# Kernel optimization log

Hardware: AMD Instinct MI355X
Metric: run time of the kernel (lower is better)

Reference implementation:

```python
import jax, jax.numpy as jnp
import numpy as np
from jax import lax


def haar_dwt2(x):
    """Single-level 2D Haar (db1) DWT matching pywt sign conventions.
    x: (..., H, W) with H, W even. Returns (cA, cH, cV, cD) each (..., H/2, W/2).
    pywt db1: approx = (x0+x1)/sqrt2, detail = (x0-x1)/sqrt2; dwt2 keys:
    cH='da' (detail axis -2), cV='ad' (detail axis -1).
    """
    a = x[..., 0::2, 0::2]
    b = x[..., 0::2, 1::2]
    c = x[..., 1::2, 0::2]
    d = x[..., 1::2, 1::2]
    cA = (a + b + c + d) * 0.5
    cH = (a + b - c - d) * 0.5
    cV = (a - b + c - d) * 0.5
    cD = (a - b - c + d) * 0.5
    return cA, cH, cV, cD


def wavedec2_level2_array(x):
    """pywt.wavedec2(x, 'db1', level=2) followed by pywt.coeffs_to_array.
    x: (B, C, H, W) -> (B, C, H, W) coefficient array with layout:
      [[ [[cA2, cH2],[cV2, cD2]], cH1 ],
       [ cV1,                     cD1 ]]
    """
    cA1, cH1, cV1, cD1 = haar_dwt2(x)
    cA2, cH2, cV2, cD2 = haar_dwt2(cA1)
    lvl2 = jnp.concatenate([
        jnp.concatenate([cA2, cH2], axis=-1),
        jnp.concatenate([cV2, cD2], axis=-1),
    ], axis=-2)
    top = jnp.concatenate([lvl2, cH1], axis=-1)
    bot = jnp.concatenate([cV1, cD1], axis=-1)
    return jnp.concatenate([top, bot], axis=-2)


def setup_inputs() -> dict:
    key = jax.random.key(0)
    k1, k2, k3 = jax.random.split(key, 3)
    B, C, H = 128, 3, 224
    dim, patch = 768, 16
    x = jax.random.normal(k1, (B, C, H, H), dtype=jnp.float32)
    # Conv2d default init scale ~ 1/sqrt(fan_in)
    fan_in = C * patch * patch
    W = jax.random.normal(k2, (dim, C, patch, patch), dtype=jnp.float32) / np.sqrt(fan_in)
    b = jax.random.normal(k3, (dim,), dtype=jnp.float32) / np.sqrt(fan_in)
    return {"x": x, "W": W, "b": b}


def reference(x, W, b):
    patch = W.shape[-1]
    coeffs = wavedec2_level2_array(x)  # (B, C, H, W)
    y = lax.conv_general_dilated(
        coeffs, W,
        window_strides=(patch, patch),
        padding='VALID',
        dimension_numbers=('NCHW', 'OIHW', 'NCHW'),
    ) + b[None, :, None, None]          # (B, dim, H/p, W/p)
    B, D, Hp, Wp = y.shape
    return y.reshape(B, D, Hp * Wp).transpose(0, 2, 1)  # (B, seq, dim)
```

## Files before the change

### kernel.cpp

```cpp
#include <hip/hip_runtime.h>
#include <stdint.h>

typedef __attribute__((ext_vector_type(8))) __bf16 bf16x8;
typedef __attribute__((ext_vector_type(4))) float f32x4;

__device__ __forceinline__ unsigned short f2bf(float f) {
  union { float f; unsigned int u; } v; v.f = f;
  unsigned int u = v.u;
  return (unsigned short)((u + 0x7fffu + ((u >> 16) & 1u)) >> 16);
}

__device__ __forceinline__ void async_copy16(const void* g, void* s) {
  __builtin_amdgcn_global_load_lds(
      (__attribute__((address_space(1))) void*)const_cast<void*>(g),
      (__attribute__((address_space(3))) void*)s,
      16, 0, 0);
}

#define HAAR(a, bb, cc, dd, oA, oH, oV, oD)                                    \
  oA = 0.5f * ((a + bb) + (cc + dd));                                          \
  oH = 0.5f * ((a + bb) - (cc + dd));                                          \
  oV = 0.5f * ((a - bb) + (cc - dd));                                          \
  oD = 0.5f * ((a - bb) - (cc - dd));

__global__ __launch_bounds__(256) void convw_kernel(const float* __restrict__ W,
                                                    unsigned short* __restrict__ Wb) {
  int i = blockIdx.x * 256 + threadIdx.x;
  float4 v = ((const float4*)W)[i];
  uint2 o;
  o.x = (unsigned int)f2bf(v.x) | ((unsigned int)f2bf(v.y) << 16);
  o.y = (unsigned int)f2bf(v.z) | ((unsigned int)f2bf(v.w) << 16);
  ((uint2*)Wb)[i] = o;
}

__global__ __launch_bounds__(256) void dwt2_kernel(const float* __restrict__ x,
                                                   unsigned short* __restrict__ A) {
  int tid = blockIdx.x * 256 + threadIdx.x;
  int J = tid % 56;
  int t = tid / 56;
  int I = t % 56;
  t /= 56;
  int c = t % 3;
  int b = t / 3;

  const float* xp = x + (((size_t)t * 224 + 4 * I) * 224 + 4 * J);
  float4 r0 = *(const float4*)(xp);
  float4 r1 = *(const float4*)(xp + 224);
  float4 r2 = *(const float4*)(xp + 448);
  float4 r3 = *(const float4*)(xp + 672);

  float A1[2][2], H1[2][2], V1[2][2], D1[2][2];
  HAAR(r0.x, r0.y, r1.x, r1.y, A1[0][0], H1[0][0], V1[0][0], D1[0][0]);
  HAAR(r0.z, r0.w, r1.z, r1.w, A1[0][1], H1[0][1], V1[0][1], D1[0][1]);
  HAAR(r2.x, r2.y, r3.x, r3.y, A1[1][0], H1[1][0], V1[1][0], D1[1][0]);
  HAAR(r2.z, r2.w, r3.z, r3.w, A1[1][1], H1[1][1], V1[1][1], D1[1][1]);

  auto aidx = [&](int y, int xx) -> size_t {
    int mrow = b * 196 + (y >> 4) * 14 + (xx >> 4);
    int k = c * 256 + (y & 15) * 16 + (xx & 15);
    return (size_t)mrow * 768 + (size_t)k;
  };
  auto store2 = [&](int y, int xx, float v0, float v1) {
    unsigned int p = (unsigned int)f2bf(v0) | ((unsigned int)f2bf(v1) << 16);
    *(unsigned int*)(A + aidx(y, xx)) = p;
  };

  int y0 = 2 * I, x0 = 2 * J;
  store2(y0,           112 + x0, H1[0][0], H1[0][1]);
  store2(y0 + 1,       112 + x0, H1[1][0], H1[1][1]);
  store2(112 + y0,     x0,       V1[0][0], V1[0][1]);
  store2(112 + y0 + 1, x0,       V1[1][0], V1[1][1]);
  store2(112 + y0,     112 + x0, D1[0][0], D1[0][1]);
  store2(112 + y0 + 1, 112 + x0, D1[1][0], D1[1][1]);

  float vA2, vH2, vV2, vD2;
  HAAR(A1[0][0], A1[0][1], A1[1][0], A1[1][1], vA2, vH2, vV2, vD2);
  A[aidx(I,      J)]      = f2bf(vA2);
  A[aidx(I,      56 + J)] = f2bf(vH2);
  A[aidx(56 + I, J)]      = f2bf(vV2);
  A[aidx(56 + I, 56 + J)] = f2bf(vD2);
}

__global__ __launch_bounds__(512, 4) void gemm_kernel(const unsigned short* __restrict__ A,
                                                      const unsigned short* __restrict__ Bt,
                                                      const float* __restrict__ bias,
                                                      float* __restrict__ C) {
  constexpr int K = 768, N = 768;
  constexpr int NT = 24;
  __shared__ unsigned short As[3][128 * 32];
  __shared__ unsigned short Bs[3][128 * 32];

  const int orig = blockIdx.x;
  const int tile = (orig & 7) * 147 + (orig >> 3);
  const int bm = tile / 6, bn = tile % 6;

  const int tid = threadIdx.x;
  const int lane = tid & 63;
  const int wave = tid >> 6;
  const int wr = wave >> 2, wc = wave & 3;
  const int mbase = bm * 128, nbase = bn * 128;

  f32x4 acc[4][2] = {};

  const int off0 = wave * 1024 + lane * 16;
  const int row0 = off0 >> 6;
  const int kc0 = (off0 >> 4) & 3;
  const int kcs = kc0 ^ ((row0 >> 1) & 3);
  const unsigned short* ga = A + (size_t)(mbase + row0) * K + kcs * 8;
  const unsigned short* gb = Bt + (size_t)(nbase + row0) * K + kcs * 8;

  auto stage = [&](int buf, int kt) {
    char* sa = (char*)As + buf * 8192 + wave * 1024;
    char* sb = (char*)Bs + buf * 8192 + wave * 1024;
    const int ko = kt * 32;
    async_copy16(ga + ko, sa);
    async_copy16(gb + ko, sb);
  };

  const int fr = lane & 15;
  const int kq = lane >> 4;
  const int chq = kq ^ ((fr >> 1) & 3);

  stage(0, 0);
  stage(1, 1);

#pragma unroll
  for (int kt = 0; kt < NT; ++kt) {
    if (kt < NT - 1)
      asm volatile("s_waitcnt vmcnt(2)" ::: "memory");
    else
      asm volatile("s_waitcnt vmcnt(0)" ::: "memory");
    __builtin_amdgcn_s_barrier();
    if (kt + 2 < NT) stage((kt + 2) % 3, kt + 2);

    const char* pa = (const char*)As + (kt % 3) * 8192 + (wr * 64 + fr) * 64 + chq * 16;
    const char* pb = (const char*)Bs + (kt % 3) * 8192 + (wc * 32 + fr) * 64 + chq * 16;
    bf16x8 af[4], bv[2];
#pragma unroll
    for (int mi = 0; mi < 4; ++mi) af[mi] = *(const bf16x8*)(pa + mi * 16 * 64);
#pragma unroll
    for (int ni = 0; ni < 2; ++ni) bv[ni] = *(const bf16x8*)(pb + ni * 16 * 64);
#pragma unroll
    for (int mi = 0; mi < 4; ++mi)
#pragma unroll
      for (int ni = 0; ni < 2; ++ni)
        acc[mi][ni] = __builtin_amdgcn_mfma_f32_16x16x32_bf16(af[mi], bv[ni],
                                                              acc[mi][ni], 0, 0, 0);
    asm volatile("s_waitcnt lgkmcnt(0)" ::: "memory");
  }

  const int rq = lane >> 4;
#pragma unroll
  for (int ni = 0; ni < 2; ++ni) {
    int n = nbase + wc * 32 + ni * 16 + fr;
    float bv = bias[n];
#pragma unroll
    for (int mi = 0; mi < 4; ++mi) {
      int mrow = mbase + wr * 64 + mi * 16 + rq * 4;
      f32x4 v = acc[mi][ni];
#pragma unroll
      for (int j = 0; j < 4; ++j) C[(size_t)(mrow + j) * N + n] = v[j] + bv;
    }
  }
}

extern "C" void kernel_launch(void* const* d_in, const int* in_sizes, int n_in,
                              void* d_out, int out_size, void* d_ws, size_t ws_size,
                              hipStream_t stream) {
  const float* x = (const float*)d_in[0];
  const float* W = (const float*)d_in[1];
  const float* bias = (const float*)d_in[2];
  float* out = (float*)d_out;

  unsigned short* A = (unsigned short*)d_ws;
  unsigned short* Wb = (unsigned short*)((char*)d_ws + 38535168);

  convw_kernel<<<576, 256, 0, stream>>>(W, Wb);
  dwt2_kernel<<<4704, 256, 0, stream>>>(x, A);
  gemm_kernel<<<1176, 512, 0, stream>>>(A, Wb, bias, out);
}
```

Measured before the change: 73.76 us.

## Restructure GEMM to 2-wave 32x32x16 MFMA tiles with double buffering

The GEMM block drops from 8 waves to 2. Each wave now computes a 64x128 sub-tile with 32x32x16 bf16 MFMAs instead of 16x16x32, and each thread issues four async copies per stage. The LDS pipeline goes from triple to double buffering with a full vmcnt(0) wait each iteration. The intent is higher per-wave arithmetic intensity and fewer LDS fragment loads, at the cost of less latency hiding, fewer waves per CU and more accumulator registers per thread.

```diff
diff --git a/kernel.cpp b/kernel.cpp
--- a/kernel.cpp
+++ b/kernel.cpp
@@ -3,6 +3,7 @@
 
 typedef __attribute__((ext_vector_type(8))) __bf16 bf16x8;
 typedef __attribute__((ext_vector_type(4))) float f32x4;
+typedef __attribute__((ext_vector_type(16))) float f32x16;
 
 __device__ __forceinline__ unsigned short f2bf(float f) {
   union { float f; unsigned int u; } v; v.f = f;
@@ -81,14 +82,14 @@
   A[aidx(56 + I, 56 + J)] = f2bf(vD2);
 }
 
-__global__ __launch_bounds__(512, 4) void gemm_kernel(const unsigned short* __restrict__ A,
+__global__ __launch_bounds__(128, 2) void gemm_kernel(const unsigned short* __restrict__ A,
                                                       const unsigned short* __restrict__ Bt,
                                                       const float* __restrict__ bias,
                                                       float* __restrict__ C) {
   constexpr int K = 768, N = 768;
   constexpr int NT = 24;
-  __shared__ unsigned short As[3][128 * 32];
-  __shared__ unsigned short Bs[3][128 * 32];
+  __shared__ unsigned short As[2][128 * 32];
+  __shared__ unsigned short Bs[2][128 * 32];
 
   const int orig = blockIdx.x;
   const int tile = (orig & 7) * 147 + (orig >> 3);
@@ -97,69 +98,83 @@
   const int tid = threadIdx.x;
   const int lane = tid & 63;
   const int wave = tid >> 6;
-  const int wr = wave >> 2, wc = wave & 3;
   const int mbase = bm * 128, nbase = bn * 128;
 
-  f32x4 acc[4][2] = {};
+  f32x16 acc[2][4] = {};
 
-  const int off0 = wave * 1024 + lane * 16;
-  const int row0 = off0 >> 6;
-  const int kc0 = (off0 >> 4) & 3;
-  const int kcs = kc0 ^ ((row0 >> 1) & 3);
-  const unsigned short* ga = A + (size_t)(mbase + row0) * K + kcs * 8;
-  const unsigned short* gb = Bt + (size_t)(nbase + row0) * K + kcs * 8;
+  const unsigned short* gA[4];
+  const unsigned short* gB[4];
+#pragma unroll
+  for (int i = 0; i < 4; ++i) {
+    int off = i * 2048 + wave * 1024 + lane * 16;
+    int row = off >> 6;
+    int kc = (off >> 4) & 3;
+    int kcs = kc ^ ((row >> 1) & 3);
+    gA[i] = A + (size_t)(mbase + row) * K + kcs * 8;
+    gB[i] = Bt + (size_t)(nbase + row) * K + kcs * 8;
+  }
 
   auto stage = [&](int buf, int kt) {
     char* sa = (char*)As + buf * 8192 + wave * 1024;
     char* sb = (char*)Bs + buf * 8192 + wave * 1024;
     const int ko = kt * 32;
-    async_copy16(ga + ko, sa);
-    async_copy16(gb + ko, sb);
+#pragma unroll
+    for (int i = 0; i < 4; ++i) {
+      async_copy16(gA[i] + ko, sa + i * 2048);
+      async_copy16(gB[i] + ko, sb + i * 2048);
+    }
   };
 
-  const int fr = lane & 15;
-  const int kq = lane >> 4;
-  const int chq = kq ^ ((fr >> 1) & 3);
+  const int fr = lane & 31;
+  const int kh = lane >> 5;
+  const int swz = (fr >> 1) & 3;
+  const int c0 = (kh ^ swz) * 16;
+  const int c1 = ((2 + kh) ^ swz) * 16;
 
   stage(0, 0);
-  stage(1, 1);
 
 #pragma unroll
   for (int kt = 0; kt < NT; ++kt) {
-    if (kt < NT - 1)
-      asm volatile("s_waitcnt vmcnt(2)" ::: "memory");
-    else
-      asm volatile("s_waitcnt vmcnt(0)" ::: "memory");
+    asm volatile("s_waitcnt vmcnt(0)" ::: "memory");
     __builtin_amdgcn_s_barrier();
-    if (kt + 2 < NT) stage((kt + 2) % 3, kt + 2);
+    if (kt + 1 < NT) stage((kt + 1) & 1, kt + 1);
 
-    const char* pa = (const char*)As + (kt % 3) * 8192 + (wr * 64 + fr) * 64 + chq * 16;
-    const char* pb = (const char*)Bs + (kt % 3) * 8192 + (wc * 32 + fr) * 64 + chq * 16;
-    bf16x8 af[4], bv[2];
+    const char* pa = (const char*)As + (kt & 1) * 8192 + (wave * 64 + fr) * 64;
+    const char* pb = (const char*)Bs + (kt & 1) * 8192 + fr * 64;
 #pragma unroll
-    for (int mi = 0; mi < 4; ++mi) af[mi] = *(const bf16x8*)(pa + mi * 16 * 64);
+    for (int s = 0; s < 2; ++s) {
+      const int cc = s ? c1 : c0;
+      bf16x8 af[2], bv[4];
+      af[0] = *(const bf16x8*)(pa + cc);
+      af[1] = *(const bf16x8*)(pa + 32 * 64 + cc);
+      bv[0] = *(const bf16x8*)(pb + cc);
+      bv[1] = *(const bf16x8*)(pb + 32 * 64 + cc);
+      bv[2] = *(const bf16x8*)(pb + 64 * 64 + cc);
+      bv[3] = *(const bf16x8*)(pb + 96 * 64 + cc);
 #pragma unroll
-    for (int ni = 0; ni < 2; ++ni) bv[ni] = *(const bf16x8*)(pb + ni * 16 * 64);
+      for (int mt = 0; mt < 2; ++mt)
 #pragma unroll
-    for (int mi = 0; mi < 4; ++mi)
-#pragma unroll
-      for (int ni = 0; ni < 2; ++ni)
-        acc[mi][ni] = __builtin_amdgcn_mfma_f32_16x16x32_bf16(af[mi], bv[ni],
-                                                              acc[mi][ni], 0, 0, 0);
+        for (int nt = 0; nt < 4; ++nt)
+          acc[mt][nt] = __builtin_amdgcn_mfma_f32_32x32x16_bf16(
+              af[mt], bv[nt], acc[mt][nt], 0, 0, 0);
+    }
     asm volatile("s_waitcnt lgkmcnt(0)" ::: "memory");
   }
 
-  const int rq = lane >> 4;
+  const int col = lane & 31;
+  const int rowoff = 4 * kh;
 #pragma unroll
-  for (int ni = 0; ni < 2; ++ni) {
-    int n = nbase + wc * 32 + ni * 16 + fr;
-    float bv = bias[n];
+  for (int nt = 0; nt < 4; ++nt) {
+    int n = nbase + nt * 32 + col;
+    float bb = bias[n];
 #pragma unroll
-    for (int mi = 0; mi < 4; ++mi) {
-      int mrow = mbase + wr * 64 + mi * 16 + rq * 4;
-      f32x4 v = acc[mi][ni];
+    for (int mt = 0; mt < 2; ++mt) {
+      f32x16 v = acc[mt][nt];
 #pragma unroll
-      for (int j = 0; j < 4; ++j) C[(size_t)(mrow + j) * N + n] = v[j] + bv;
+      for (int r = 0; r < 16; ++r) {
+        int mrow = mbase + wave * 64 + mt * 32 + (r & 3) + 8 * (r >> 2) + rowoff;
+        C[(size_t)mrow * N + n] = v[r] + bb;
+      }
     }
   }
 }
@@ -177,5 +192,5 @@
 
   convw_kernel<<<576, 256, 0, stream>>>(W, Wb);
   dwt2_kernel<<<4704, 256, 0, stream>>>(x, A);
-  gemm_kernel<<<1176, 512, 0, stream>>>(A, Wb, bias, out);
+  gemm_kernel<<<1176, 128, 0, stream>>>(A, Wb, bias, out);
 }
```

After: 83.82 us. +13.6%, slower.
